# Kernel optimization log

Hardware: AMD Instinct MI355X
Metric: run time of the kernel (lower is better)

The kernel has to match this reference:

```python
import jax, jax.numpy as jnp
import numpy as np

N = 100_000
E = 3_200_000
IN_DIM = 2
HID = 64
NUM_LAYERS = 3


def setup_inputs() -> dict:
    key = jax.random.key(0)
    ks = jax.random.split(key, 16)
    feat = jax.random.normal(ks[0], (N, IN_DIM), dtype=jnp.float32)
    src = jax.random.randint(ks[1], (E,), 0, N, dtype=jnp.int32)
    dst = jax.random.randint(ks[2], (E,), 0, N, dtype=jnp.int32)
    u_mask = jnp.zeros((N,), dtype=bool).at[jnp.arange(0, 10)].set(True)
    v_mask = jnp.zeros((N,), dtype=bool).at[jnp.arange(10, 20)].set(True)
    inp = {"feat": feat, "src": src, "dst": dst, "u_mask": u_mask, "v_mask": v_mask}
    dims = [IN_DIM] + [HID] * NUM_LAYERS
    ki = 3
    for l in range(NUM_LAYERS):
        d_in = dims[l]
        inp[f"W1_{l}"] = jax.random.normal(ks[ki], (d_in, HID), dtype=jnp.float32) * (1.0 / np.sqrt(d_in)); ki += 1
        inp[f"b1_{l}"] = jnp.zeros((HID,), dtype=jnp.float32)
        inp[f"W2_{l}"] = jax.random.normal(ks[ki], (HID, HID), dtype=jnp.float32) * (1.0 / np.sqrt(HID)); ki += 1
        inp[f"b2_{l}"] = jnp.zeros((HID,), dtype=jnp.float32)
    return inp


def _gin_layer(h, src, dst, W1, b1, W2, b2, n_nodes):
    # GINConv(sum, eps=0): h' = MLP(h + sum_{j->i} h_j)
    agg = jax.ops.segment_sum(h[src], dst, num_segments=n_nodes)  # [N, d]
    z = h + agg
    z = jax.nn.relu(z @ W1 + b1)
    z = z @ W2 + b2
    return jax.nn.relu(z)  # module applies relu after conv


def _masked_means(h, u_mask, v_mask):
    other_mask = ~(u_mask | v_mask)
    masks = jnp.stack([u_mask, v_mask, other_mask]).astype(h.dtype)  # [3, N]
    counts = masks.sum(axis=1)                                      # [3]
    sums = masks @ h                                                # [3, H]
    means = jnp.where(counts[:, None] > 0,
                      sums / jnp.maximum(counts, 1.0)[:, None],
                      jnp.zeros_like(sums))
    return means.reshape(-1)  # [3*H] = [h_u | h_v | h_other]


def reference(feat, src, dst, u_mask, v_mask,
              W1_0, b1_0, W2_0, b2_0,
              W1_1, b1_1, W2_1, b2_1,
              W1_2, b1_2, W2_2, b2_2):
    n_nodes = feat.shape[0]
    params = [(W1_0, b1_0, W2_0, b2_0), (W1_1, b1_1, W2_1, b2_1), (W1_2, b1_2, W2_2, b2_2)]
    h = feat
    parts = []
    for (W1, b1, W2, b2) in params:
        h = _gin_layer(h, src, dst, W1, b1, W2, b2, n_nodes)
        parts.append(_masked_means(h, u_mask, v_mask))
    return jnp.concatenate(parts)  # (num_layers * 3 * hidden_dim,)
```

## Files before the change

### kernel.cpp

```cpp
#include <hip/hip_runtime.h>

#define HID 64
#define G_LOG 7
#define G_SZ 128
#define NBKT_MAX 1024
#define STAGE_MAX 6144

typedef float f32x4 __attribute__((ext_vector_type(4)));
typedef short bf16x8 __attribute__((ext_vector_type(8)));

__device__ __forceinline__ float bf2f(unsigned int u) {
    union { unsigned int i; float f; } c; c.i = u << 16; return c.f;
}
__device__ __forceinline__ unsigned short f2bf(float f) {
    union { float f; unsigned int i; } c; c.f = f;
    unsigned int r = (c.i + 0x7FFFu + ((c.i >> 16) & 1u)) >> 16;
    return (unsigned short)r;
}
__device__ __forceinline__ unsigned int pack2(float a, float b) {
    return (unsigned int)f2bf(a) | ((unsigned int)f2bf(b) << 16);
}

__global__ void detect_mask_kernel(const unsigned char* __restrict__ u,
                                   int* __restrict__ flag)
{
    *flag = (u[1] != 0) ? 1 : 0;
}

__device__ __forceinline__ int mask_at(const void* m, int n, int is_u8)
{
    return is_u8 ? (((const unsigned char*)m)[n] != 0)
                 : (((const int*)m)[n] != 0);
}

__global__ __launch_bounds__(256) void count_masks_kernel(
    const void* __restrict__ u, const void* __restrict__ v,
    const int* __restrict__ flag, int* __restrict__ counts, int N)
{
    const int is_u8 = *flag;
    int tid = blockIdx.x * blockDim.x + threadIdx.x;
    int stride = gridDim.x * blockDim.x;
    int cu = 0, cv = 0, co = 0;
    for (int n = tid; n < N; n += stride) {
        int bu = mask_at(u, n, is_u8), bv = mask_at(v, n, is_u8);
        cu += bu; cv += bv; co += ((bu | bv) ^ 1);
    }
    atomicAdd(&counts[0], cu);
    atomicAdd(&counts[1], cv);
    atomicAdd(&counts[2], co);
}

__global__ __launch_bounds__(1024) void bucket_hist_kernel(
    const int* __restrict__ dst, int* __restrict__ bktCount, int E, int nbkt)
{
    __shared__ int lh[NBKT_MAX];
    const int bdim = blockDim.x;
    for (int i = threadIdx.x; i < nbkt; i += bdim) lh[i] = 0;
    __syncthreads();
    const int chunk = (E + gridDim.x - 1) / gridDim.x;
    const int c0 = blockIdx.x * chunk;
    const int c1 = min(E, c0 + chunk);
    for (int e = c0 + threadIdx.x; e < c1; e += bdim)
        atomicAdd(&lh[dst[e] >> G_LOG], 1);
    __syncthreads();
    for (int i = threadIdx.x; i < nbkt; i += bdim)
        if (lh[i]) atomicAdd(&bktCount[i], lh[i]);
}

__global__ __launch_bounds__(1024) void bucket_scan_kernel(
    const int* __restrict__ bktCount, int* __restrict__ bktBase,
    int* __restrict__ bktCursor, int nbkt)
{
    __shared__ int s[NBKT_MAX];
    const int t = threadIdx.x;
    int v = (t < nbkt) ? bktCount[t] : 0;
    s[t] = v;
    __syncthreads();
    for (int off = 1; off < NBKT_MAX; off <<= 1) {
        int x = (t >= off) ? s[t - off] : 0;
        __syncthreads();
        s[t] += x;
        __syncthreads();
    }
    if (t < nbkt) {
        int excl = s[t] - v;
        bktBase[t] = excl;
        bktCursor[t] = excl;
        if (t == nbkt - 1) bktBase[nbkt] = s[t];
    }
}

__global__ __launch_bounds__(1024) void binning_kernel(
    const int* __restrict__ src, const int* __restrict__ dst,
    int* __restrict__ bktCursor, unsigned int* __restrict__ packed,
    int E, int nbkt)
{
    __shared__ int lh[NBKT_MAX];
    __shared__ int lbase[NBKT_MAX];
    __shared__ int lcur[NBKT_MAX];
    const int bdim = blockDim.x;
    for (int i = threadIdx.x; i < nbkt; i += bdim) { lh[i] = 0; lcur[i] = 0; }
    __syncthreads();
    const int chunk = (E + gridDim.x - 1) / gridDim.x;
    const int c0 = blockIdx.x * chunk;
    const int c1 = min(E, c0 + chunk);
    for (int e = c0 + threadIdx.x; e < c1; e += bdim)
        atomicAdd(&lh[dst[e] >> G_LOG], 1);
    __syncthreads();
    for (int i = threadIdx.x; i < nbkt; i += bdim) {
        int h = lh[i];
        lbase[i] = h ? atomicAdd(&bktCursor[i], h) : 0;
    }
    __syncthreads();
    for (int e = c0 + threadIdx.x; e < c1; e += bdim) {
        int d = dst[e];
        int b = d >> G_LOG;
        int r = atomicAdd(&lcur[b], 1);
        packed[lbase[b] + r] =
            (unsigned int)src[e] | ((unsigned int)(d & (G_SZ - 1)) << 20);
    }
}

__global__ __launch_bounds__(512) void bucket_csr_kernel(
    const unsigned int* __restrict__ packed, const int* __restrict__ bktBase,
    int* __restrict__ row_ptr, int* __restrict__ csr_src, int N, int E)
{
    __shared__ int ncount[G_SZ];
    __shared__ int sc[G_SZ];
    __shared__ int ncur[G_SZ];
    __shared__ int stage[STAGE_MAX];
    const int b = blockIdx.x;
    const int t = threadIdx.x;
    const int bdim = blockDim.x;
    const int beg = bktBase[b], end = bktBase[b + 1];
    const int cnt = end - beg;

    if (t < G_SZ) ncount[t] = 0;
    __syncthreads();
    for (int i = beg + t; i < end; i += bdim)
        atomicAdd(&ncount[(packed[i] >> 20) & (G_SZ - 1)], 1);
    __syncthreads();
    if (t < G_SZ) sc[t] = ncount[t];
    __syncthreads();
    for (int off = 1; off < G_SZ; off <<= 1) {
        int x = 0;
        if (t < G_SZ && t >= off) x = sc[t - off];
        __syncthreads();
        if (t < G_SZ) sc[t] += x;
        __syncthreads();
    }
    if (t < G_SZ) {
        int excl = sc[t] - ncount[t];
        ncur[t] = excl;
        int node = (b << G_LOG) + t;
        if (node < N) row_ptr[node] = beg + excl;
    }
    if (b == 0 && t == 0) row_ptr[N] = E;
    __syncthreads();

    if (cnt <= STAGE_MAX) {
        for (int i = beg + t; i < end; i += bdim) {
            unsigned int p = packed[i];
            int dl = (p >> 20) & (G_SZ - 1);
            int r = atomicAdd(&ncur[dl], 1);
            stage[r] = (int)(p & 0xFFFFFu);
        }
        __syncthreads();
        for (int i = t; i < cnt; i += bdim) csr_src[beg + i] = stage[i];
    } else {
        for (int i = beg + t; i < end; i += bdim) {
            unsigned int p = packed[i];
            int dl = (p >> 20) & (G_SZ - 1);
            int r = atomicAdd(&ncur[dl], 1);
            csr_src[beg + r] = (int)(p & 0xFFFFFu);
        }
    }
}

__global__ __launch_bounds__(256) void gather64_kernel(
    const unsigned short* __restrict__ h, const int* __restrict__ row_ptr,
    const int* __restrict__ csr_src, unsigned short* __restrict__ agg, int N)
{
    const int lane = threadIdx.x & 63;
    const int slot = lane >> 3;
    const int chunk = lane & 7;
    const int wave = (blockIdx.x * blockDim.x + threadIdx.x) >> 6;
    const int nwaves = (gridDim.x * blockDim.x) >> 6;

    for (int n = wave; n < N; n += nwaves) {
        const int beg = row_ptr[n], end = row_ptr[n + 1];
        float acc[8];
#pragma unroll
        for (int j = 0; j < 8; j++) acc[j] = 0.0f;

        for (int i = beg + slot; i < end; i += 8) {
            int s = csr_src[i];
            uint4 hv = *reinterpret_cast<const uint4*>(h + (size_t)s * HID + chunk * 8);
            acc[0] += bf2f(hv.x & 0xFFFFu); acc[1] += bf2f(hv.x >> 16);
            acc[2] += bf2f(hv.y & 0xFFFFu); acc[3] += bf2f(hv.y >> 16);
            acc[4] += bf2f(hv.z & 0xFFFFu); acc[5] += bf2f(hv.z >> 16);
            acc[6] += bf2f(hv.w & 0xFFFFu); acc[7] += bf2f(hv.w >> 16);
        }
#pragma unroll
        for (int off = 8; off < 64; off <<= 1) {
#pragma unroll
            for (int j = 0; j < 8; j++) acc[j] += __shfl_xor(acc[j], off, 64);
        }
        if (lane < 8) {
            unsigned int w0 = pack2(acc[0], acc[1]);
            unsigned int w1 = pack2(acc[2], acc[3]);
            unsigned int w2 = pack2(acc[4], acc[5]);
            unsigned int w3 = pack2(acc[6], acc[7]);
            uint4 o = {w0, w1, w2, w3};
            *reinterpret_cast<uint4*>(agg + (size_t)n * HID + lane * 8) = o;
        }
    }
}

__device__ __forceinline__ void load_wfrags(const float* __restrict__ W,
                                            int lg, int ln, bf16x8 wf[2][4])
{
#pragma unroll
    for (int kb = 0; kb < 2; kb++)
#pragma unroll
        for (int jb = 0; jb < 4; jb++) {
            bf16x8 w;
#pragma unroll
            for (int j = 0; j < 8; j++)
                w[j] = (short)f2bf(W[(kb * 32 + lg * 8 + j) * HID + jb * 16 + ln]);
            wf[kb][jb] = w;
        }
}

__device__ __forceinline__ bf16x8 zfrag_add(const unsigned short* __restrict__ h,
                                            const unsigned short* __restrict__ agg,
                                            size_t off)
{
    uint4 hv = *reinterpret_cast<const uint4*>(h + off);
    uint4 av = *reinterpret_cast<const uint4*>(agg + off);
    bf16x8 r;
    r[0] = (short)f2bf(bf2f(hv.x & 0xFFFFu) + bf2f(av.x & 0xFFFFu));
    r[1] = (short)f2bf(bf2f(hv.x >> 16) + bf2f(av.x >> 16));
    r[2] = (short)f2bf(bf2f(hv.y & 0xFFFFu) + bf2f(av.y & 0xFFFFu));
    r[3] = (short)f2bf(bf2f(hv.y >> 16) + bf2f(av.y >> 16));
    r[4] = (short)f2bf(bf2f(hv.z & 0xFFFFu) + bf2f(av.z & 0xFFFFu));
    r[5] = (short)f2bf(bf2f(hv.z >> 16) + bf2f(av.z >> 16));
    r[6] = (short)f2bf(bf2f(hv.w & 0xFFFFu) + bf2f(av.w & 0xFFFFu));
    r[7] = (short)f2bf(bf2f(hv.w >> 16) + bf2f(av.w >> 16));
    return r;
}

__global__ __launch_bounds__(256) void gin64_mfma_kernel(
    const unsigned short* __restrict__ h, const unsigned short* __restrict__ agg,
    const float* __restrict__ W1, const float* __restrict__ b1,
    const float* __restrict__ W2, const float* __restrict__ b2,
    unsigned short* __restrict__ out, int N)
{
    __shared__ __align__(16) unsigned short ytile[4][64 * 18];
    __shared__ __align__(16) unsigned short otile[4][16 * 72];

    const int lane = threadIdx.x & 63;
    const int wid = threadIdx.x >> 6;
    const int lg = lane >> 4, ln = lane & 15;

    bf16x8 w1f[2][4], w2f[2][4];
    load_wfrags(W1, lg, ln, w1f);
    load_wfrags(W2, lg, ln, w2f);
    float b1v[4], b2v[4];
#pragma unroll
    for (int jb = 0; jb < 4; jb++) {
        b1v[jb] = b1[jb * 16 + ln];
        b2v[jb] = b2[jb * 16 + ln];
    }

    const int nb = (blockIdx.x * 4 + wid) * 16;
    if (nb >= N) return;

    const int nodeA = min(nb + ln, N - 1);
    bf16x8 a0 = zfrag_add(h, agg, (size_t)nodeA * HID + 0 * 32 + lg * 8);
    bf16x8 a1 = zfrag_add(h, agg, (size_t)nodeA * HID + 1 * 32 + lg * 8);

    unsigned short* yt = ytile[wid];
#pragma unroll
    for (int jb = 0; jb < 4; jb++) {
        f32x4 acc = {0.f, 0.f, 0.f, 0.f};
        acc = __builtin_amdgcn_mfma_f32_16x16x32_bf16(a0, w1f[0][jb], acc, 0, 0, 0);
        acc = __builtin_amdgcn_mfma_f32_16x16x32_bf16(a1, w1f[1][jb], acc, 0, 0, 0);
#pragma unroll
        for (int r = 0; r < 4; r++) {
            float v = fmaxf(acc[r] + b1v[jb], 0.0f);
            yt[(jb * 16 + ln) * 18 + lg * 4 + r] = f2bf(v);
        }
    }
    __builtin_amdgcn_s_waitcnt(0);

    bf16x8 a2[2];
#pragma unroll
    for (int kb = 0; kb < 2; kb++) {
        bf16x8 t;
#pragma unroll
        for (int j = 0; j < 8; j++)
            t[j] = (short)yt[(kb * 32 + lg * 8 + j) * 18 + ln];
        a2[kb] = t;
    }

    unsigned short* ot = otile[wid];
#pragma unroll
    for (int jb = 0; jb < 4; jb++) {
        f32x4 acc = {0.f, 0.f, 0.f, 0.f};
        acc = __builtin_amdgcn_mfma_f32_16x16x32_bf16(a2[0], w2f[0][jb], acc, 0, 0, 0);
        acc = __builtin_amdgcn_mfma_f32_16x16x32_bf16(a2[1], w2f[1][jb], acc, 0, 0, 0);
#pragma unroll
        for (int r = 0; r < 4; r++) {
            float v = fmaxf(acc[r] + b2v[jb], 0.0f);
            ot[(lg * 4 + r) * 72 + jb * 16 + ln] = f2bf(v);
        }
    }
    __builtin_amdgcn_s_waitcnt(0);

    const int node2 = nb + (lane >> 2);
    if (node2 < N) {
        const unsigned short* sp = ot + (lane >> 2) * 72 + (lane & 3) * 16;
        uint4 o0 = *reinterpret_cast<const uint4*>(sp);
        uint4 o1 = *reinterpret_cast<const uint4*>(sp + 8);
        unsigned short* gp = out + (size_t)node2 * HID + (lane & 3) * 16;
        *reinterpret_cast<uint4*>(gp) = o0;
        *reinterpret_cast<uint4*>(gp + 8) = o1;
    }
}

__global__ __launch_bounds__(256) void mm64_relu_mfma_kernel(
    const unsigned short* __restrict__ in,
    const float* __restrict__ W, const float* __restrict__ b,
    unsigned short* __restrict__ out, int N)
{
    __shared__ __align__(16) unsigned short otile[4][16 * 72];

    const int lane = threadIdx.x & 63;
    const int wid = threadIdx.x >> 6;
    const int lg = lane >> 4, ln = lane & 15;

    bf16x8 wf[2][4];
    load_wfrags(W, lg, ln, wf);
    float bv[4];
#pragma unroll
    for (int jb = 0; jb < 4; jb++) bv[jb] = b[jb * 16 + ln];

    const int nb = (blockIdx.x * 4 + wid) * 16;
    if (nb >= N) return;

    const int nodeA = min(nb + ln, N - 1);
    bf16x8 a0 = *reinterpret_cast<const bf16x8*>(in + (size_t)nodeA * HID + 0 * 32 + lg * 8);
    bf16x8 a1 = *reinterpret_cast<const bf16x8*>(in + (size_t)nodeA * HID + 1 * 32 + lg * 8);

    unsigned short* ot = otile[wid];
#pragma unroll
    for (int jb = 0; jb < 4; jb++) {
        f32x4 acc = {0.f, 0.f, 0.f, 0.f};
        acc = __builtin_amdgcn_mfma_f32_16x16x32_bf16(a0, wf[0][jb], acc, 0, 0, 0);
        acc = __builtin_amdgcn_mfma_f32_16x16x32_bf16(a1, wf[1][jb], acc, 0, 0, 0);
#pragma unroll
        for (int r = 0; r < 4; r++) {
            float v = fmaxf(acc[r] + bv[jb], 0.0f);
            ot[(lg * 4 + r) * 72 + jb * 16 + ln] = f2bf(v);
        }
    }
    __builtin_amdgcn_s_waitcnt(0);

    const int node2 = nb + (lane >> 2);
    if (node2 < N) {
        const unsigned short* sp = ot + (lane >> 2) * 72 + (lane & 3) * 16;
        uint4 o0 = *reinterpret_cast<const uint4*>(sp);
        uint4 o1 = *reinterpret_cast<const uint4*>(sp + 8);
        unsigned short* gp = out + (size_t)node2 * HID + (lane & 3) * 16;
        *reinterpret_cast<uint4*>(gp) = o0;
        *reinterpret_cast<uint4*>(gp + 8) = o1;
    }
}

__global__ __launch_bounds__(256) void mlp2_y1_kernel(
    const float* __restrict__ feat, const int* __restrict__ row_ptr,
    const int* __restrict__ csr_src,
    const float* __restrict__ W1, const float* __restrict__ b1,
    unsigned short* __restrict__ out, int N)
{
    __shared__ float W1s[2 * HID];
    __shared__ float b1s[HID];
    const int tid = threadIdx.x;
    if (tid < 2 * HID) W1s[tid] = W1[tid];
    if (tid < HID) b1s[tid] = b1[tid];
    __syncthreads();

    const int stride = gridDim.x * 256;
    for (int node = blockIdx.x * 256 + tid; node < N; node += stride) {
        float2 f = *reinterpret_cast<const float2*>(&feat[(size_t)node * 2]);
        float z0 = f.x, z1 = f.y;
        const int beg = row_ptr[node], end = row_ptr[node + 1];
        int i = beg;
        for (; i + 3 < end; i += 4) {
            float2 g0 = *reinterpret_cast<const float2*>(&feat[(size_t)csr_src[i + 0] * 2]);
            float2 g1 = *reinterpret_cast<const float2*>(&feat[(size_t)csr_src[i + 1] * 2]);
            float2 g2 = *reinterpret_cast<const float2*>(&feat[(size_t)csr_src[i + 2] * 2]);
            float2 g3 = *reinterpret_cast<const float2*>(&feat[(size_t)csr_src[i + 3] * 2]);
            z0 += (g0.x + g1.x) + (g2.x + g3.x);
            z1 += (g0.y + g1.y) + (g2.y + g3.y);
        }
        for (; i < end; ++i) {
            float2 g = *reinterpret_cast<const float2*>(&feat[(size_t)csr_src[i] * 2]);
            z0 += g.x; z1 += g.y;
        }
        uint4* op = reinterpret_cast<uint4*>(out + (size_t)node * HID);
#pragma unroll
        for (int jc = 0; jc < 4; jc++) {
            unsigned int w[8];
#pragma unroll
            for (int p = 0; p < 8; p++) {
                int j0 = jc * 16 + 2 * p, j1 = j0 + 1;
                float v0 = fmaxf(b1s[j0] + z0 * W1s[j0] + z1 * W1s[HID + j0], 0.f);
                float v1 = fmaxf(b1s[j1] + z0 * W1s[j1] + z1 * W1s[HID + j1], 0.f);
                w[p] = pack2(v0, v1);
            }
            uint4 o0 = {w[0], w[1], w[2], w[3]};
            uint4 o1 = {w[4], w[5], w[6], w[7]};
            op[jc * 2 + 0] = o0;
            op[jc * 2 + 1] = o1;
        }
    }
}

__global__ __launch_bounds__(256) void masked_reduce_kernel(
    const unsigned short* __restrict__ h, const void* __restrict__ u,
    const void* __restrict__ v, const int* __restrict__ flag,
    float* __restrict__ sums, int N)
{
    __shared__ float ls[3][HID];
    const int tid = threadIdx.x;
    const int is_u8 = *flag;
    const int f8 = tid & 7;
    const int nloc = tid >> 3;

    if (tid < 3 * HID) ls[tid / HID][tid % HID] = 0.0f;
    __syncthreads();

    float su[8], sv[8], so[8];
#pragma unroll
    for (int j = 0; j < 8; j++) { su[j] = 0.f; sv[j] = 0.f; so[j] = 0.f; }

    for (int base = blockIdx.x * 32; base < N; base += gridDim.x * 32) {
        int n = base + nloc;
        if (n < N) {
            uint4 hv = *reinterpret_cast<const uint4*>(h + (size_t)n * HID + f8 * 8);
            float x[8];
            x[0] = bf2f(hv.x & 0xFFFFu); x[1] = bf2f(hv.x >> 16);
            x[2] = bf2f(hv.y & 0xFFFFu); x[3] = bf2f(hv.y >> 16);
            x[4] = bf2f(hv.z & 0xFFFFu); x[5] = bf2f(hv.z >> 16);
            x[6] = bf2f(hv.w & 0xFFFFu); x[7] = bf2f(hv.w >> 16);
            int bu = mask_at(u, n, is_u8), bv = mask_at(v, n, is_u8);
            if (bu) {
#pragma unroll
                for (int j = 0; j < 8; j++) su[j] += x[j];
            }
            if (bv) {
#pragma unroll
                for (int j = 0; j < 8; j++) sv[j] += x[j];
            }
            if (!(bu | bv)) {
#pragma unroll
                for (int j = 0; j < 8; j++) so[j] += x[j];
            }
        }
    }

#pragma unroll
    for (int off = 8; off < 64; off <<= 1) {
#pragma unroll
        for (int j = 0; j < 8; j++) {
            su[j] += __shfl_xor(su[j], off, 64);
            sv[j] += __shfl_xor(sv[j], off, 64);
            so[j] += __shfl_xor(so[j], off, 64);
        }
    }
    if ((tid & 63) < 8) {
        const int f0 = (tid & 7) * 8;
#pragma unroll
        for (int j = 0; j < 8; j++) {
            atomicAdd(&ls[0][f0 + j], su[j]);
            atomicAdd(&ls[1][f0 + j], sv[j]);
            atomicAdd(&ls[2][f0 + j], so[j]);
        }
    }
    __syncthreads();
    if (tid < 3 * HID) {
        float vsum = ls[tid / HID][tid % HID];
        if (vsum != 0.0f) atomicAdd(&sums[tid], vsum);
    }
}

__global__ void finalize_kernel(const float* __restrict__ sums,
                                const int* __restrict__ counts,
                                float* __restrict__ out)
{
    int i = blockIdx.x * blockDim.x + threadIdx.x;
    if (i >= 3 * 3 * HID) return;
    int g = (i / HID) % 3;
    float c = (float)counts[g];
    out[i] = (c > 0.0f) ? sums[i] / fmaxf(c, 1.0f) : 0.0f;
}

extern "C" void kernel_launch(void* const* d_in, const int* in_sizes, int n_in,
                              void* d_out, int out_size, void* d_ws, size_t ws_size,
                              hipStream_t stream)
{
    const float* feat = (const float*)d_in[0];
    const int* src = (const int*)d_in[1];
    const int* dst = (const int*)d_in[2];
    const void* um = d_in[3];
    const void* vm = d_in[4];
    const float* W1_0 = (const float*)d_in[5];
    const float* b1_0 = (const float*)d_in[6];
    const float* W2_0 = (const float*)d_in[7];
    const float* b2_0 = (const float*)d_in[8];
    const float* W1_1 = (const float*)d_in[9];
    const float* b1_1 = (const float*)d_in[10];
    const float* W2_1 = (const float*)d_in[11];
    const float* b2_1 = (const float*)d_in[12];
    const float* W1_2 = (const float*)d_in[13];
    const float* b1_2 = (const float*)d_in[14];
    const float* W2_2 = (const float*)d_in[15];
    const float* b2_2 = (const float*)d_in[16];

    const int N = in_sizes[0] / 2;
    const int E = in_sizes[1];
    const int nbkt = (N + G_SZ - 1) >> G_LOG;

    unsigned short* bufA = (unsigned short*)d_ws;
    unsigned short* bufB = bufA + (size_t)N * HID;
    unsigned short* bufC = bufB + (size_t)N * HID;
    unsigned int* packed = (unsigned int*)(bufC + (size_t)N * HID);
    int* csr_src = (int*)(packed + E);
    int* row_ptr = csr_src + E;
    int* bktCount = row_ptr + (N + 1);
    int* bktBase = bktCount + (NBKT_MAX + 1);
    int* bktCursor = bktBase + (NBKT_MAX + 1);
    float* sums = (float*)(bktCursor + NBKT_MAX);
    int* counts = (int*)(sums + 3 * 3 * HID);
    int* flag = counts + 3;

    const int mfma_grid = (N + 63) / 64;

    hipMemsetAsync(sums, 0, (3 * 3 * HID) * sizeof(float) + 3 * sizeof(int), stream);
    hipMemsetAsync(bktCount, 0, (NBKT_MAX + 1) * sizeof(int), stream);
    detect_mask_kernel<<<1, 1, 0, stream>>>((const unsigned char*)um, flag);
    count_masks_kernel<<<64, 256, 0, stream>>>(um, vm, flag, counts, N);

    bucket_hist_kernel<<<256, 1024, 0, stream>>>(dst, bktCount, E, nbkt);
    bucket_scan_kernel<<<1, 1024, 0, stream>>>(bktCount, bktBase, bktCursor, nbkt);
    binning_kernel<<<256, 1024, 0, stream>>>(src, dst, bktCursor, packed, E, nbkt);
    bucket_csr_kernel<<<nbkt, 512, 0, stream>>>(packed, bktBase, row_ptr, csr_src, N, E);

    mlp2_y1_kernel<<<(N + 255) / 256, 256, 0, stream>>>(feat, row_ptr, csr_src,
                                                        W1_0, b1_0, bufB, N);
    mm64_relu_mfma_kernel<<<mfma_grid, 256, 0, stream>>>(bufB, W2_0, b2_0, bufA, N);
    masked_reduce_kernel<<<512, 256, 0, stream>>>(bufA, um, vm, flag, sums + 0 * 3 * HID, N);

    gather64_kernel<<<2048, 256, 0, stream>>>(bufA, row_ptr, csr_src, bufB, N);
    gin64_mfma_kernel<<<mfma_grid, 256, 0, stream>>>(bufA, bufB, W1_1, b1_1,
                                                     W2_1, b2_1, bufC, N);
    masked_reduce_kernel<<<512, 256, 0, stream>>>(bufC, um, vm, flag, sums + 1 * 3 * HID, N);

    gather64_kernel<<<2048, 256, 0, stream>>>(bufC, row_ptr, csr_src, bufB, N);
    gin64_mfma_kernel<<<mfma_grid, 256, 0, stream>>>(bufC, bufB, W1_2, b1_2,
                                                     W2_2, b2_2, bufA, N);
    masked_reduce_kernel<<<512, 256, 0, stream>>>(bufA, um, vm, flag, sums + 2 * 3 * HID, N);

    finalize_kernel<<<1, 576, 0, stream>>>(sums, counts, (float*)d_out);
}
```

Measured before the change: 322.7 us.

## Store node features in four 16-wide feature slices to shrink gather working set

Hidden features are now stored as four planar slices of 16 bf16 values per node instead of contiguous 64-wide rows. The gather kernel splits its waves into four passes, one per slice, and each wave covers 32 edges per iteration, so each pass gathers from a 3.2 MB slice that fits in cache better. The producer, GIN and reduce kernels are updated to read and write the sliced layout, and high-half bf16 unpacking uses a mask instead of a shift. The cost is that each 32-byte row fetch uses less of a cache line, CSR indices are read four times, and more shuffle reduction steps are needed per node.

```diff
diff --git a/kernel.cpp b/kernel.cpp
--- a/kernel.cpp
+++ b/kernel.cpp
@@ -12,6 +12,9 @@
 __device__ __forceinline__ float bf2f(unsigned int u) {
     union { unsigned int i; float f; } c; c.i = u << 16; return c.f;
 }
+__device__ __forceinline__ float bf2f_hi(unsigned int u) {
+    union { unsigned int i; float f; } c; c.i = u & 0xFFFF0000u; return c.f;
+}
 __device__ __forceinline__ unsigned short f2bf(float f) {
     union { float f; unsigned int i; } c; c.f = f;
     unsigned int r = (c.i + 0x7FFFu + ((c.i >> 16) & 1u)) >> 16;
@@ -20,6 +23,7 @@
 __device__ __forceinline__ unsigned int pack2(float a, float b) {
     return (unsigned int)f2bf(a) | ((unsigned int)f2bf(b) << 16);
 }
+
 
 __global__ void detect_mask_kernel(const unsigned char* __restrict__ u,
                                    int* __restrict__ flag)
@@ -177,42 +181,48 @@
     }
 }
 
-__global__ __launch_bounds__(256) void gather64_kernel(
+__global__ __launch_bounds__(256) void gather_sliced_kernel(
     const unsigned short* __restrict__ h, const int* __restrict__ row_ptr,
     const int* __restrict__ csr_src, unsigned short* __restrict__ agg, int N)
 {
     const int lane = threadIdx.x & 63;
-    const int slot = lane >> 3;
-    const int chunk = lane & 7;
-    const int wave = (blockIdx.x * blockDim.x + threadIdx.x) >> 6;
-    const int nwaves = (gridDim.x * blockDim.x) >> 6;
-
-    for (int n = wave; n < N; n += nwaves) {
+    const int slot = lane >> 1;
+    const int half = lane & 1;
+    const int w = (blockIdx.x * blockDim.x + threadIdx.x) >> 6;
+    const int total_waves = (gridDim.x * blockDim.x) >> 6;
+    const int wpp = total_waves >> 2;
+    const int pass = w / wpp;
+    const int w0 = w - pass * wpp;
+
+    const unsigned short* hs = h + (size_t)pass * N * 16;
+    unsigned short* as = agg + (size_t)pass * N * 16;
+
+    for (int n = w0; n < N; n += wpp) {
         const int beg = row_ptr[n], end = row_ptr[n + 1];
         float acc[8];
 #pragma unroll
         for (int j = 0; j < 8; j++) acc[j] = 0.0f;
 
-        for (int i = beg + slot; i < end; i += 8) {
+        for (int i = beg + slot; i < end; i += 32) {
             int s = csr_src[i];
-            uint4 hv = *reinterpret_cast<const uint4*>(h + (size_t)s * HID + chunk * 8);
-            acc[0] += bf2f(hv.x & 0xFFFFu); acc[1] += bf2f(hv.x >> 16);
-            acc[2] += bf2f(hv.y & 0xFFFFu); acc[3] += bf2f(hv.y >> 16);
-            acc[4] += bf2f(hv.z & 0xFFFFu); acc[5] += bf2f(hv.z >> 16);
-            acc[6] += bf2f(hv.w & 0xFFFFu); acc[7] += bf2f(hv.w >> 16);
-        }
-#pragma unroll
-        for (int off = 8; off < 64; off <<= 1) {
+            uint4 hv = *reinterpret_cast<const uint4*>(hs + (size_t)s * 16 + half * 8);
+            acc[0] += bf2f(hv.x & 0xFFFFu); acc[1] += bf2f_hi(hv.x);
+            acc[2] += bf2f(hv.y & 0xFFFFu); acc[3] += bf2f_hi(hv.y);
+            acc[4] += bf2f(hv.z & 0xFFFFu); acc[5] += bf2f_hi(hv.z);
+            acc[6] += bf2f(hv.w & 0xFFFFu); acc[7] += bf2f_hi(hv.w);
+        }
+#pragma unroll
+        for (int off = 2; off < 64; off <<= 1) {
 #pragma unroll
             for (int j = 0; j < 8; j++) acc[j] += __shfl_xor(acc[j], off, 64);
         }
-        if (lane < 8) {
-            unsigned int w0 = pack2(acc[0], acc[1]);
-            unsigned int w1 = pack2(acc[2], acc[3]);
-            unsigned int w2 = pack2(acc[4], acc[5]);
-            unsigned int w3 = pack2(acc[6], acc[7]);
-            uint4 o = {w0, w1, w2, w3};
-            *reinterpret_cast<uint4*>(agg + (size_t)n * HID + lane * 8) = o;
+        if (lane < 2) {
+            unsigned int w0p = pack2(acc[0], acc[1]);
+            unsigned int w1p = pack2(acc[2], acc[3]);
+            unsigned int w2p = pack2(acc[4], acc[5]);
+            unsigned int w3p = pack2(acc[6], acc[7]);
+            uint4 o = {w0p, w1p, w2p, w3p};
+            *reinterpret_cast<uint4*>(as + (size_t)n * 16 + lane * 8) = o;
         }
     }
 }
@@ -232,21 +242,22 @@
         }
 }
 
-__device__ __forceinline__ bf16x8 zfrag_add(const unsigned short* __restrict__ h,
-                                            const unsigned short* __restrict__ agg,
-                                            size_t off)
-{
+__device__ __forceinline__ bf16x8 zfrag_add_sliced(
+    const unsigned short* __restrict__ h, const unsigned short* __restrict__ agg,
+    int node, int f0, int N)
+{
+    size_t off = (size_t)(f0 >> 4) * N * 16 + (size_t)node * 16 + (f0 & 15);
     uint4 hv = *reinterpret_cast<const uint4*>(h + off);
     uint4 av = *reinterpret_cast<const uint4*>(agg + off);
     bf16x8 r;
     r[0] = (short)f2bf(bf2f(hv.x & 0xFFFFu) + bf2f(av.x & 0xFFFFu));
-    r[1] = (short)f2bf(bf2f(hv.x >> 16) + bf2f(av.x >> 16));
+    r[1] = (short)f2bf(bf2f_hi(hv.x) + bf2f_hi(av.x));
     r[2] = (short)f2bf(bf2f(hv.y & 0xFFFFu) + bf2f(av.y & 0xFFFFu));
-    r[3] = (short)f2bf(bf2f(hv.y >> 16) + bf2f(av.y >> 16));
+    r[3] = (short)f2bf(bf2f_hi(hv.y) + bf2f_hi(av.y));
     r[4] = (short)f2bf(bf2f(hv.z & 0xFFFFu) + bf2f(av.z & 0xFFFFu));
-    r[5] = (short)f2bf(bf2f(hv.z >> 16) + bf2f(av.z >> 16));
+    r[5] = (short)f2bf(bf2f_hi(hv.z) + bf2f_hi(av.z));
     r[6] = (short)f2bf(bf2f(hv.w & 0xFFFFu) + bf2f(av.w & 0xFFFFu));
-    r[7] = (short)f2bf(bf2f(hv.w >> 16) + bf2f(av.w >> 16));
+    r[7] = (short)f2bf(bf2f_hi(hv.w) + bf2f_hi(av.w));
     return r;
 }
 
@@ -277,8 +288,8 @@
     if (nb >= N) return;
 
     const int nodeA = min(nb + ln, N - 1);
-    bf16x8 a0 = zfrag_add(h, agg, (size_t)nodeA * HID + 0 * 32 + lg * 8);
-    bf16x8 a1 = zfrag_add(h, agg, (size_t)nodeA * HID + 1 * 32 + lg * 8);
+    bf16x8 a0 = zfrag_add_sliced(h, agg, nodeA, 0 * 32 + lg * 8, N);
+    bf16x8 a1 = zfrag_add_sliced(h, agg, nodeA, 1 * 32 + lg * 8, N);
 
     unsigned short* yt = ytile[wid];
 #pragma unroll
@@ -323,7 +334,7 @@
         const unsigned short* sp = ot + (lane >> 2) * 72 + (lane & 3) * 16;
         uint4 o0 = *reinterpret_cast<const uint4*>(sp);
         uint4 o1 = *reinterpret_cast<const uint4*>(sp + 8);
-        unsigned short* gp = out + (size_t)node2 * HID + (lane & 3) * 16;
+        unsigned short* gp = out + (size_t)(lane & 3) * N * 16 + (size_t)node2 * 16;
         *reinterpret_cast<uint4*>(gp) = o0;
         *reinterpret_cast<uint4*>(gp + 8) = o1;
     }
@@ -372,7 +383,7 @@
         const unsigned short* sp = ot + (lane >> 2) * 72 + (lane & 3) * 16;
         uint4 o0 = *reinterpret_cast<const uint4*>(sp);
         uint4 o1 = *reinterpret_cast<const uint4*>(sp + 8);
-        unsigned short* gp = out + (size_t)node2 * HID + (lane & 3) * 16;
+        unsigned short* gp = out + (size_t)(lane & 3) * N * 16 + (size_t)node2 * 16;
         *reinterpret_cast<uint4*>(gp) = o0;
         *reinterpret_cast<uint4*>(gp + 8) = o1;
     }
@@ -442,6 +453,8 @@
     if (tid < 3 * HID) ls[tid / HID][tid % HID] = 0.0f;
     __syncthreads();
 
+    const unsigned short* hsl = h + (size_t)(f8 >> 1) * N * 16 + (f8 & 1) * 8;
+
     float su[8], sv[8], so[8];
 #pragma unroll
     for (int j = 0; j < 8; j++) { su[j] = 0.f; sv[j] = 0.f; so[j] = 0.f; }
@@ -449,12 +462,12 @@
     for (int base = blockIdx.x * 32; base < N; base += gridDim.x * 32) {
         int n = base + nloc;
         if (n < N) {
-            uint4 hv = *reinterpret_cast<const uint4*>(h + (size_t)n * HID + f8 * 8);
+            uint4 hv = *reinterpret_cast<const uint4*>(hsl + (size_t)n * 16);
             float x[8];
-            x[0] = bf2f(hv.x & 0xFFFFu); x[1] = bf2f(hv.x >> 16);
-            x[2] = bf2f(hv.y & 0xFFFFu); x[3] = bf2f(hv.y >> 16);
-            x[4] = bf2f(hv.z & 0xFFFFu); x[5] = bf2f(hv.z >> 16);
-            x[6] = bf2f(hv.w & 0xFFFFu); x[7] = bf2f(hv.w >> 16);
+            x[0] = bf2f(hv.x & 0xFFFFu); x[1] = bf2f_hi(hv.x);
+            x[2] = bf2f(hv.y & 0xFFFFu); x[3] = bf2f_hi(hv.y);
+            x[4] = bf2f(hv.z & 0xFFFFu); x[5] = bf2f_hi(hv.z);
+            x[6] = bf2f(hv.w & 0xFFFFu); x[7] = bf2f_hi(hv.w);
             int bu = mask_at(u, n, is_u8), bv = mask_at(v, n, is_u8);
             if (bu) {
 #pragma unroll
@@ -563,12 +576,12 @@
     mm64_relu_mfma_kernel<<<mfma_grid, 256, 0, stream>>>(bufB, W2_0, b2_0, bufA, N);
     masked_reduce_kernel<<<512, 256, 0, stream>>>(bufA, um, vm, flag, sums + 0 * 3 * HID, N);
 
-    gather64_kernel<<<2048, 256, 0, stream>>>(bufA, row_ptr, csr_src, bufB, N);
+    gather_sliced_kernel<<<2048, 256, 0, stream>>>(bufA, row_ptr, csr_src, bufB, N);
     gin64_mfma_kernel<<<mfma_grid, 256, 0, stream>>>(bufA, bufB, W1_1, b1_1,
                                                      W2_1, b2_1, bufC, N);
     masked_reduce_kernel<<<512, 256, 0, stream>>>(bufC, um, vm, flag, sums + 1 * 3 * HID, N);
 
-    gather64_kernel<<<2048, 256, 0, stream>>>(bufC, row_ptr, csr_src, bufB, N);
+    gather_sliced_kernel<<<2048, 256, 0, stream>>>(bufC, row_ptr, csr_src, bufB, N);
     gin64_mfma_kernel<<<mfma_grid, 256, 0, stream>>>(bufC, bufB, W1_2, b1_2,
                                                      W2_2, b2_2, bufA, N);
     masked_reduce_kernel<<<512, 256, 0, stream>>>(bufA, um, vm, flag, sums + 2 * 3 * HID, N);
```

New measurement: 585.9 us. +81.6%, slower.
